# Kernel tuning notes

Hardware: AMD Instinct MI355X
Metric: run time of the kernel (lower is better)

Reference implementation:

```python
import jax, jax.numpy as jnp
import numpy as np

NUM_HEAD = 16
MODEL_DIM = 1024
K_DIM = MODEL_DIM // NUM_HEAD
LN_EPS = 1e-5


def setup_inputs() -> dict:
    key = jax.random.key(0)
    ks = jax.random.split(key, 9)
    B, N, D = 4, 2048, MODEL_DIM
    scale = 1.0 / np.sqrt(D)
    return {
        "q": jax.random.normal(ks[0], (B, N, D), dtype=jnp.float32),
        "k": jax.random.normal(ks[1], (B, N, D), dtype=jnp.float32),
        "v": jax.random.normal(ks[2], (B, N, D), dtype=jnp.float32),
        "Wq": jax.random.normal(ks[3], (D, D), dtype=jnp.float32) * scale,
        "Wk": jax.random.normal(ks[4], (D, D), dtype=jnp.float32) * scale,
        "Wv": jax.random.normal(ks[5], (D, D), dtype=jnp.float32) * scale,
        "Wo": jax.random.normal(ks[6], (D, D), dtype=jnp.float32) * scale,
        "gamma": jnp.ones((D,), dtype=jnp.float32),
        "beta": jnp.zeros((D,), dtype=jnp.float32),
    }


def reference(q, k, v, Wq, Wk, Wv, Wo, gamma, beta):
    B, N, D = q.shape
    H, Dh = NUM_HEAD, K_DIM
    # QKV projections (torch Linear: x @ W.T), then split heads -> [B,H,N,Dh]
    qs = (q @ Wq.T).reshape(B, N, H, Dh).transpose(0, 2, 1, 3)
    ks = (k @ Wk.T).reshape(B, N, H, Dh).transpose(0, 2, 1, 3)
    vs = (v @ Wv.T).reshape(B, N, H, Dh).transpose(0, 2, 1, 3)
    # scaled dot-product attention
    scores = jnp.einsum("bhqd,bhkd->bhqk", qs, ks) / jnp.sqrt(jnp.float32(Dh))
    probs = jax.nn.softmax(scores, axis=-1)
    attn = jnp.einsum("bhqk,bhkd->bhqd", probs, vs)
    # merge heads and output projection
    attn = attn.transpose(0, 2, 1, 3).reshape(B, N, D)
    out = attn @ Wo.T + q  # residual
    # LayerNorm
    mu = jnp.mean(out, axis=-1, keepdims=True)
    var = jnp.var(out, axis=-1, keepdims=True)
    out = (out - mu) * jax.lax.rsqrt(var + LN_EPS) * gamma + beta
    return out
```

## Files before the change

### kernel.cpp

```cpp
#include <hip/hip_runtime.h>
#include <cstdint>
#include <math.h>

typedef __bf16 bf16x8 __attribute__((ext_vector_type(8)));
typedef float f32x2 __attribute__((ext_vector_type(2)));
typedef float f32x4 __attribute__((ext_vector_type(4)));
typedef float f32x16 __attribute__((ext_vector_type(16)));
typedef int i32x2 __attribute__((ext_vector_type(2)));
typedef unsigned u32x4 __attribute__((ext_vector_type(4)));
typedef unsigned short u16;

#define B_ 4
#define N_ 2048
#define D_ 1024
#define H_ 16
#define DH_ 64
#define M_ (B_*N_)

#define QSCALE (0.125f * 1.44269504088896f)

typedef const void __attribute__((address_space(1))) gvoid;
typedef void __attribute__((address_space(3))) lvoid;

__device__ __forceinline__ void gload16(const void* g, void* l) {
  __builtin_amdgcn_global_load_lds((gvoid*)g, (lvoid*)l, 16, 0, 0);
}

__device__ __forceinline__ u16 cvt_bf(float f) {
  __bf16 h = (__bf16)f;
  return *(u16*)&h;
}

__device__ __forceinline__ unsigned cvt_pk(float lo, float hi) {
  unsigned r;
  asm("v_cvt_pk_bf16_f32 %0, %1, %2" : "=v"(r) : "v"(lo), "v"(hi));
  return r;
}

__device__ __forceinline__ i32x2 pl32swap(unsigned a, unsigned b) {
  return __builtin_amdgcn_permlane32_swap((int)a, (int)b, false, false);
}

__device__ __forceinline__ f32x2 pk_add(f32x2 a, f32x2 b) {
  f32x2 d;
  asm("v_pk_add_f32 %0, %1, %2" : "=v"(d) : "v"(a), "v"(b));
  return d;
}
__device__ __forceinline__ f32x2 pk_mul(f32x2 a, f32x2 b) {
  f32x2 d;
  asm("v_pk_mul_f32 %0, %1, %2" : "=v"(d) : "v"(a), "v"(b));
  return d;
}

__global__ __launch_bounds__(256) void cast_w(
    const float* __restrict__ a, const float* __restrict__ b,
    const float* __restrict__ c, const float* __restrict__ e,
    u16* __restrict__ oa, u16* __restrict__ ob, u16* __restrict__ oc, u16* __restrict__ oe) {
  const int nw = (D_*D_)/4;
  int i = blockIdx.x * 256 + threadIdx.x;
  const float* s; u16* d;
  if (i < nw)        { s = a; d = oa; }
  else if (i < 2*nw) { s = b; d = ob; i -= nw; }
  else if (i < 3*nw) { s = c; d = oc; i -= 2*nw; }
  else               { s = e; d = oe; i -= 3*nw; }
  float4 x = ((const float4*)s)[i];
  ushort4 y;
  y.x = cvt_bf(x.x); y.y = cvt_bf(x.y); y.z = cvt_bf(x.z); y.w = cvt_bf(x.w);
  ((ushort4*)d)[i] = y;
}

__global__ __launch_bounds__(256) void gemm_qkv(
    const float* __restrict__ Aq, const float* __restrict__ Ak, const float* __restrict__ Av,
    const u16* __restrict__ Wq, const u16* __restrict__ Wk, const u16* __restrict__ Wv,
    u16* __restrict__ Oq, u16* __restrict__ Ok, u16* __restrict__ Ov)
{
  __shared__ __align__(16) float As32[128*64];
  __shared__ __align__(16) u16 Bs[128*64];
  const int z = blockIdx.z;
  const float* A = (z == 0) ? Aq : (z == 1) ? Ak : Av;
  const u16* W  = (z == 0) ? Wq : (z == 1) ? Wk : Wv;
  u16* obf      = (z == 0) ? Oq : (z == 1) ? Ok : Ov;
  const float oscale = (z == 0) ? QSCALE : 1.0f;

  const int t = threadIdx.x;
  const int lane = t & 63;
  const int w = t >> 6;
  const int wr = w >> 1, wc = w & 1;
  const int m0 = blockIdx.x * 128;
  const int n0 = blockIdx.y * 128;
  f32x4 acc[4][4] = {};

  const int srow = t >> 3;
  const int scb = (t & 7) ^ (srow & 7);
  const int arow = t >> 4;
  const int asb  = (t & 15) ^ arow;

  const int fr = lane & 15;
  const int fg = lane >> 4;
  const int fs7 = fr & 7;

  for (int k0 = 0; k0 < 1024; k0 += 64) {
#pragma unroll
    for (int p = 0; p < 4; ++p)
      gload16(W + (size_t)(n0 + p*32 + srow)*1024 + k0 + scb*8, &Bs[(p*256 + t)*8]);
#pragma unroll
    for (int p = 0; p < 8; ++p)
      gload16(A + (size_t)(m0 + p*16 + arow)*1024 + k0 + asb*4, &As32[(p*256 + t)*4]);
    __syncthreads();
#pragma unroll
    for (int ks = 0; ks < 2; ++ks) {
      bf16x8 af[4], bfr[4];
#pragma unroll
      for (int i = 0; i < 4; ++i) {
        int ra = wr*64 + i*16 + fr;
        int b0 = (ks*4 + fg) * 2;
        int r15 = ra & 15;
        f32x4 lo = *(const f32x4*)&As32[ra*64 + ((b0 ^ r15) * 4)];
        f32x4 hi = *(const f32x4*)&As32[ra*64 + (((b0 + 1) ^ r15) * 4)];
        u32x4 pk = { cvt_pk(lo.x, lo.y), cvt_pk(lo.z, lo.w),
                     cvt_pk(hi.x, hi.y), cvt_pk(hi.z, hi.w) };
        af[i] = __builtin_bit_cast(bf16x8, pk);
        int rb = wc*64 + i*16 + fr;
        bfr[i] = *(const bf16x8*)&Bs[rb*64 + (((ks*4 + fg) ^ fs7) * 8)];
      }
#pragma unroll
      for (int i = 0; i < 4; ++i)
#pragma unroll
        for (int j = 0; j < 4; ++j)
          acc[i][j] = __builtin_amdgcn_mfma_f32_16x16x32_bf16(af[i], bfr[j], acc[i][j], 0, 0, 0);
    }
    __syncthreads();
  }

#pragma unroll
  for (int i = 0; i < 4; ++i) {
#pragma unroll
    for (int j = 0; j < 4; ++j) {
#pragma unroll
      for (int jj = 0; jj < 4; ++jj) {
        int row = m0 + wr*64 + i*16 + fg*4 + jj;
        int col = n0 + wc*64 + j*16 + fr;
        float val = acc[i][j][jj];
        int b = row >> 11, n = row & 2047, h = col >> 6, dh = col & 63;
        if (z != 2) {
          obf[(((size_t)(b*H_ + h))*N_ + n)*DH_ + dh] = cvt_bf(val * oscale);
        } else {
          obf[(((size_t)(b*H_ + h))*DH_ + dh)*N_ + n] = cvt_bf(val);
        }
      }
    }
  }
}

__global__ __launch_bounds__(256) void gemm_out(
    const u16* __restrict__ A, const u16* __restrict__ W,
    const float* __restrict__ resid, float* __restrict__ ofp)
{
  __shared__ __align__(16) u16 As[128*64];
  __shared__ __align__(16) u16 Bs[128*64];
  const int t = threadIdx.x;
  const int lane = t & 63;
  const int w = t >> 6;
  const int wr = w >> 1, wc = w & 1;
  const int m0 = blockIdx.x * 128;
  const int n0 = blockIdx.y * 128;
  f32x4 acc[4][4] = {};

  const int srow = t >> 3;
  const int scb = (t & 7) ^ (srow & 7);
  const int fr = lane & 15;
  const int fg = lane >> 4;
  const int fs7 = fr & 7;

  for (int k0 = 0; k0 < 1024; k0 += 64) {
#pragma unroll
    for (int p = 0; p < 4; ++p) {
      int r = p*32 + srow;
      gload16(A + (size_t)(m0 + r)*1024 + k0 + scb*8, &As[(p*256 + t)*8]);
      gload16(W + (size_t)(n0 + r)*1024 + k0 + scb*8, &Bs[(p*256 + t)*8]);
    }
    __syncthreads();
#pragma unroll
    for (int ks = 0; ks < 2; ++ks) {
      bf16x8 af[4], bfr[4];
#pragma unroll
      for (int i = 0; i < 4; ++i) {
        int ra = wr*64 + i*16 + fr;
        af[i]  = *(const bf16x8*)&As[ra*64 + (((ks*4 + fg) ^ fs7) * 8)];
        int rb = wc*64 + i*16 + fr;
        bfr[i] = *(const bf16x8*)&Bs[rb*64 + (((ks*4 + fg) ^ fs7) * 8)];
      }
#pragma unroll
      for (int i = 0; i < 4; ++i)
#pragma unroll
        for (int j = 0; j < 4; ++j)
          acc[i][j] = __builtin_amdgcn_mfma_f32_16x16x32_bf16(af[i], bfr[j], acc[i][j], 0, 0, 0);
    }
    __syncthreads();
  }

#pragma unroll
  for (int i = 0; i < 4; ++i)
#pragma unroll
    for (int j = 0; j < 4; ++j)
#pragma unroll
      for (int jj = 0; jj < 4; ++jj) {
        int row = m0 + wr*64 + i*16 + fg*4 + jj;
        int col = n0 + wc*64 + j*16 + fr;
        size_t idx = (size_t)row*1024 + col;
        ofp[idx] = acc[i][j][jj] + resid[idx];
      }
}

__device__ __forceinline__ f32x2 sp2(const f32x16& S, int i) {
  f32x2 r; r.x = S[2*i]; r.y = S[2*i + 1]; return r;
}
__device__ __forceinline__ void exp2v(f32x16& S) {
#pragma unroll
  for (int r = 0; r < 16; ++r) S[r] = __builtin_amdgcn_exp2f(S[r]);
}
__device__ __forceinline__ f32x2 sumtree(const f32x16& S0, const f32x16& S1) {
  f32x2 a0 = pk_add(sp2(S0,0), sp2(S0,1));
  f32x2 a1 = pk_add(sp2(S0,2), sp2(S0,3));
  f32x2 a2 = pk_add(sp2(S0,4), sp2(S0,5));
  f32x2 a3 = pk_add(sp2(S0,6), sp2(S0,7));
  f32x2 b0 = pk_add(sp2(S1,0), sp2(S1,1));
  f32x2 b1 = pk_add(sp2(S1,2), sp2(S1,3));
  f32x2 b2 = pk_add(sp2(S1,4), sp2(S1,5));
  f32x2 b3 = pk_add(sp2(S1,6), sp2(S1,7));
  a0 = pk_add(a0, a1); a2 = pk_add(a2, a3);
  b0 = pk_add(b0, b1); b2 = pk_add(b2, b3);
  a0 = pk_add(a0, a2); b0 = pk_add(b0, b2);
  return pk_add(a0, b0);
}
__device__ __forceinline__ void buildP(const f32x16& S, bf16x8* pf) {
  unsigned w0 = cvt_pk(S[0], S[1]),  w1 = cvt_pk(S[2], S[3]);
  unsigned w2 = cvt_pk(S[4], S[5]),  w3 = cvt_pk(S[6], S[7]);
  i32x2 A2 = pl32swap(w0, w2), B2 = pl32swap(w1, w3);
  u32x4 f0 = { (unsigned)A2.x, (unsigned)B2.x, (unsigned)A2.y, (unsigned)B2.y };
  pf[0] = __builtin_bit_cast(bf16x8, f0);
  unsigned w4 = cvt_pk(S[8], S[9]),   w5 = cvt_pk(S[10], S[11]);
  unsigned w6 = cvt_pk(S[12], S[13]), w7 = cvt_pk(S[14], S[15]);
  i32x2 C2 = pl32swap(w4, w6), D2 = pl32swap(w5, w7);
  u32x4 f1 = { (unsigned)C2.x, (unsigned)D2.x, (unsigned)C2.y, (unsigned)D2.y };
  pf[1] = __builtin_bit_cast(bf16x8, f1);
}

__global__ __launch_bounds__(256, 2) void flash_attn(
    const u16* __restrict__ Qs, const u16* __restrict__ Ks,
    const u16* __restrict__ VTs, u16* __restrict__ ctx)
{
  __shared__ __align__(16) u16 Klds[2][128*64];
  __shared__ __align__(16) u16 Vlds[2][64*128];
  const int t = threadIdx.x;
  const int lane = t & 63;
  const int w = t >> 6;
  const int l31 = lane & 31;
  const int h = lane >> 5;
  const int bh = blockIdx.x;
  const int q0 = blockIdx.y * 256 + w * 64;
  const u16* Qbh = Qs  + (size_t)bh * N_ * DH_;
  const u16* Kbh = Ks  + (size_t)bh * N_ * DH_;
  const u16* Vbh = VTs + (size_t)bh * DH_ * N_;

  bf16x8 qfA[4], qfB[4];
#pragma unroll
  for (int dd = 0; dd < 4; ++dd) {
    qfA[dd] = *(const bf16x8*)&Qbh[(size_t)(q0 + l31)*64 + dd*16 + h*8];
    qfB[dd] = *(const bf16x8*)&Qbh[(size_t)(q0 + 32 + l31)*64 + dd*16 + h*8];
  }

  f32x2 lA = {0.f, 0.f}, lB = {0.f, 0.f};
  f32x16 OA0 = {}, OA1 = {}, OB0 = {}, OB1 = {};

  const int krow = t >> 3;
  const int kcb  = (t & 7) ^ (krow & 7);
  const int vrow = t >> 4;
  const int vcb  = (t & 15) ^ vrow;
  const u16* ksrc = Kbh + (size_t)krow*64 + kcb*8;
  const u16* vsrc = Vbh + (size_t)vrow*N_ + vcb*8;

  auto stage = [&](int buf, int kv) {
#pragma unroll
    for (int p = 0; p < 4; ++p)
      gload16(ksrc + (size_t)(kv + p*32)*64, &Klds[buf][(p*256 + t)*8]);
#pragma unroll
    for (int p = 0; p < 4; ++p)
      gload16(vsrc + kv + (size_t)(p*16)*N_, &Vlds[buf][(p*256 + t)*8]);
  };

  const int l7 = l31 & 7;
  const int l15 = l31 & 15;

  stage(0, 0);
  __syncthreads();
  int cur = 0;

  for (int kv0 = 0; kv0 < N_; kv0 += 128) {
    if (kv0 + 128 < N_) stage(cur ^ 1, kv0 + 128);

#pragma unroll
    for (int c = 0; c < 2; ++c) {
      const int kb = c * 64;
      bf16x8 kf0[4], kf1[4];
#pragma unroll
      for (int dd = 0; dd < 4; ++dd) {
        int cb = ((dd*2 + h) ^ l7) * 8;
        kf0[dd] = *(const bf16x8*)&Klds[cur][(kb + l31)*64 + cb];
        kf1[dd] = *(const bf16x8*)&Klds[cur][(kb + 32 + l31)*64 + cb];
      }
      bf16x8 vf0[4], vf1[4];
#pragma unroll
      for (int ks = 0; ks < 4; ++ks) {
        int kc = (c*8 + ks*2 + h) ^ l15;
        vf0[ks] = *(const bf16x8*)&Vlds[cur][l31*128 + kc*8];
        vf1[ks] = *(const bf16x8*)&Vlds[cur][(32 + l31)*128 + kc*8];
      }

      f32x16 SA0 = {}, SA1 = {}, SB0 = {}, SB1 = {};
#pragma unroll
      for (int dd = 0; dd < 4; ++dd) {
        SA0 = __builtin_amdgcn_mfma_f32_32x32x16_bf16(kf0[dd], qfA[dd], SA0, 0, 0, 0);
        SA1 = __builtin_amdgcn_mfma_f32_32x32x16_bf16(kf1[dd], qfA[dd], SA1, 0, 0, 0);
      }
#pragma unroll
      for (int dd = 0; dd < 4; ++dd) {
        SB0 = __builtin_amdgcn_mfma_f32_32x32x16_bf16(kf0[dd], qfB[dd], SB0, 0, 0, 0);
        SB1 = __builtin_amdgcn_mfma_f32_32x32x16_bf16(kf1[dd], qfB[dd], SB1, 0, 0, 0);
      }

      exp2v(SA0); exp2v(SA1);
      bf16x8 pfA[4];
      buildP(SA0, &pfA[0]);
      buildP(SA1, &pfA[2]);

#pragma unroll
      for (int ks = 0; ks < 4; ++ks) {
        OA0 = __builtin_amdgcn_mfma_f32_32x32x16_bf16(vf0[ks], pfA[ks], OA0, 0, 0, 0);
        OA1 = __builtin_amdgcn_mfma_f32_32x32x16_bf16(vf1[ks], pfA[ks], OA1, 0, 0, 0);
      }
      lA = pk_add(lA, sumtree(SA0, SA1));

      exp2v(SB0); exp2v(SB1);
      bf16x8 pfB[4];
      buildP(SB0, &pfB[0]);
      buildP(SB1, &pfB[2]);
#pragma unroll
      for (int ks = 0; ks < 4; ++ks) {
        OB0 = __builtin_amdgcn_mfma_f32_32x32x16_bf16(vf0[ks], pfB[ks], OB0, 0, 0, 0);
        OB1 = __builtin_amdgcn_mfma_f32_32x32x16_bf16(vf1[ks], pfB[ks], OB1, 0, 0, 0);
      }
      lB = pk_add(lB, sumtree(SB0, SB1));
    }

    __syncthreads();
    cur ^= 1;
  }

  int b = bh >> 4, hh = bh & 15;
  {
    float lps = lA.x + lA.y;
    i32x2 lsw = pl32swap(__float_as_uint(lps), __float_as_uint(lps));
    float ltot = __uint_as_float((unsigned)lsw.x) + __uint_as_float((unsigned)lsw.y);
    float linv = __builtin_amdgcn_rcpf(ltot);
    f32x2 li2; li2.x = linv; li2.y = linv;
    unsigned* crow = (unsigned*)(ctx + ((size_t)b*N_ + (q0 + l31))*D_ + hh*64);
#pragma unroll
    for (int rp = 0; rp < 8; ++rp) {
      int r = rp*2;
      int d0 = (r & 3) + 8*(r >> 2) + 4*h;
      f32x2 o0 = pk_mul(sp2(OA0, rp), li2);
      f32x2 o1 = pk_mul(sp2(OA1, rp), li2);
      crow[d0 >> 1]        = cvt_pk(o0.x, o0.y);
      crow[(d0 + 32) >> 1] = cvt_pk(o1.x, o1.y);
    }
  }
  {
    float lps = lB.x + lB.y;
    i32x2 lsw = pl32swap(__float_as_uint(lps), __float_as_uint(lps));
    float ltot = __uint_as_float((unsigned)lsw.x) + __uint_as_float((unsigned)lsw.y);
    float linv = __builtin_amdgcn_rcpf(ltot);
    f32x2 li2; li2.x = linv; li2.y = linv;
    unsigned* crow = (unsigned*)(ctx + ((size_t)b*N_ + (q0 + 32 + l31))*D_ + hh*64);
#pragma unroll
    for (int rp = 0; rp < 8; ++rp) {
      int r = rp*2;
      int d0 = (r & 3) + 8*(r >> 2) + 4*h;
      f32x2 o0 = pk_mul(sp2(OB0, rp), li2);
      f32x2 o1 = pk_mul(sp2(OB1, rp), li2);
      crow[d0 >> 1]        = cvt_pk(o0.x, o0.y);
      crow[(d0 + 32) >> 1] = cvt_pk(o1.x, o1.y);
    }
  }
}

__global__ __launch_bounds__(256) void ln_fwd(float* __restrict__ io,
    const float* __restrict__ gamma, const float* __restrict__ beta)
{
  __shared__ float red[4];
  const int t = threadIdx.x;
  const int lane = t & 63, w = t >> 6;
  float4* row = (float4*)(io + (size_t)blockIdx.x * 1024);
  float4 x = row[t];
  float s = x.x + x.y + x.z + x.w;
#pragma unroll
  for (int m = 1; m < 64; m <<= 1) s += __shfl_xor(s, m);
  if (lane == 0) red[w] = s;
  __syncthreads();
  float mean = (red[0] + red[1] + red[2] + red[3]) * (1.f/1024.f);
  __syncthreads();
  float dx0 = x.x - mean, dx1 = x.y - mean, dx2 = x.z - mean, dx3 = x.w - mean;
  float sq = dx0*dx0 + dx1*dx1 + dx2*dx2 + dx3*dx3;
#pragma unroll
  for (int m = 1; m < 64; m <<= 1) sq += __shfl_xor(sq, m);
  if (lane == 0) red[w] = sq;
  __syncthreads();
  float var = (red[0] + red[1] + red[2] + red[3]) * (1.f/1024.f);
  float rstd = rsqrtf(var + 1e-5f);
  float4 g = ((const float4*)gamma)[t];
  float4 bb = ((const float4*)beta)[t];
  float4 y;
  y.x = dx0*rstd*g.x + bb.x;
  y.y = dx1*rstd*g.y + bb.y;
  y.z = dx2*rstd*g.z + bb.z;
  y.w = dx3*rstd*g.w + bb.w;
  row[t] = y;
}

extern "C" void kernel_launch(void* const* d_in, const int* in_sizes, int n_in,
                              void* d_out, int out_size, void* d_ws, size_t ws_size,
                              hipStream_t stream) {
  const float* q     = (const float*)d_in[0];
  const float* k     = (const float*)d_in[1];
  const float* v     = (const float*)d_in[2];
  const float* Wq    = (const float*)d_in[3];
  const float* Wk    = (const float*)d_in[4];
  const float* Wv    = (const float*)d_in[5];
  const float* Wo    = (const float*)d_in[6];
  const float* gamma = (const float*)d_in[7];
  const float* beta  = (const float*)d_in[8];
  float* out = (float*)d_out;

  char* ws = (char*)d_ws;
  const size_t MB = 1024*1024;
  u16* Wqb = (u16*)(ws + 0*MB);
  u16* Wkb = (u16*)(ws + 2*MB);
  u16* Wvb = (u16*)(ws + 4*MB);
  u16* Wob = (u16*)(ws + 6*MB);
  u16* Qs  = (u16*)(ws + 8*MB);
  u16* Ks  = (u16*)(ws + 24*MB);
  u16* VTs = (u16*)(ws + 40*MB);
  u16* ctx = (u16*)(ws + 56*MB);

  const int nw4 = 4*((D_*D_)/4);
  cast_w<<<nw4/256, 256, 0, stream>>>(Wq, Wk, Wv, Wo, Wqb, Wkb, Wvb, Wob);

  dim3 gproj(M_/128, D_/128, 3);
  gemm_qkv<<<gproj, 256, 0, stream>>>(q, k, v, Wqb, Wkb, Wvb, Qs, Ks, VTs);

  flash_attn<<<dim3(B_*H_, N_/256), 256, 0, stream>>>(Qs, Ks, VTs, ctx);

  gemm_out<<<dim3(M_/128, D_/128), 256, 0, stream>>>(ctx, Wob, q, out);

  ln_fwd<<<M_, 256, 0, stream>>>(out, gamma, beta);
}
```

Before: 209.5 us.

## Prefetch next K tile in QKV GEMM and convert activations to bf16 before LDS

Measured after the change: 223.6 us. +6.8%, slower.

```diff
diff --git a/kernel.cpp b/kernel.cpp
--- a/kernel.cpp
+++ b/kernel.cpp
@@ -74,8 +74,8 @@
     const u16* __restrict__ Wq, const u16* __restrict__ Wk, const u16* __restrict__ Wv,
     u16* __restrict__ Oq, u16* __restrict__ Ok, u16* __restrict__ Ov)
 {
-  __shared__ __align__(16) float As32[128*64];
-  __shared__ __align__(16) u16 Bs[128*64];
+  __shared__ __align__(16) u16 As[128*64];
+  __shared__ __align__(16) u16 Bs[2][128*64];
   const int z = blockIdx.z;
   const float* A = (z == 0) ? Aq : (z == 1) ? Ak : Av;
   const u16* W  = (z == 0) ? Wq : (z == 1) ? Wk : Wv;
@@ -90,38 +90,64 @@
   const int n0 = blockIdx.y * 128;
   f32x4 acc[4][4] = {};
 
+  const int arow0 = t >> 3;
+  const int acb   = t & 7;
+  const float* asrc = A + (size_t)(m0 + arow0)*1024 + acb*8;
   const int srow = t >> 3;
-  const int scb = (t & 7) ^ (srow & 7);
-  const int arow = t >> 4;
-  const int asb  = (t & 15) ^ arow;
+  const int scb  = (t & 7) ^ (srow & 7);
+  const u16* wsrc = W + (size_t)(n0 + srow)*1024 + scb*8;
 
   const int fr = lane & 15;
   const int fg = lane >> 4;
   const int fs7 = fr & 7;
 
+  float4 areg[8];
+  auto aload = [&](int k0) {
+#pragma unroll
+    for (int p = 0; p < 4; ++p) {
+      const float* s = asrc + (size_t)(p*32)*1024 + k0;
+      areg[2*p]   = *(const float4*)s;
+      areg[2*p+1] = *(const float4*)(s + 4);
+    }
+  };
+  auto awrite = [&]() {
+#pragma unroll
+    for (int p = 0; p < 4; ++p) {
+      int row = p*32 + arow0;
+      u32x4 pk = { cvt_pk(areg[2*p].x,   areg[2*p].y),
+                   cvt_pk(areg[2*p].z,   areg[2*p].w),
+                   cvt_pk(areg[2*p+1].x, areg[2*p+1].y),
+                   cvt_pk(areg[2*p+1].z, areg[2*p+1].w) };
+      *(u32x4*)&As[row*64 + ((acb ^ (row & 7)) * 8)] = pk;
+    }
+  };
+  auto wstage = [&](int buf, int k0) {
+#pragma unroll
+    for (int p = 0; p < 4; ++p)
+      gload16(wsrc + (size_t)(p*32)*1024 + k0, &Bs[buf][(p*256 + t)*8]);
+  };
+
+  aload(0);
+  wstage(0, 0);
+  awrite();
+  __syncthreads();
+  int cur = 0;
+
   for (int k0 = 0; k0 < 1024; k0 += 64) {
-#pragma unroll
-    for (int p = 0; p < 4; ++p)
-      gload16(W + (size_t)(n0 + p*32 + srow)*1024 + k0 + scb*8, &Bs[(p*256 + t)*8]);
-#pragma unroll
-    for (int p = 0; p < 8; ++p)
-      gload16(A + (size_t)(m0 + p*16 + arow)*1024 + k0 + asb*4, &As32[(p*256 + t)*4]);
-    __syncthreads();
+    const bool more = (k0 + 64 < 1024);
+    if (more) {
+      aload(k0 + 64);
+      wstage(cur ^ 1, k0 + 64);
+    }
 #pragma unroll
     for (int ks = 0; ks < 2; ++ks) {
       bf16x8 af[4], bfr[4];
 #pragma unroll
       for (int i = 0; i < 4; ++i) {
         int ra = wr*64 + i*16 + fr;
-        int b0 = (ks*4 + fg) * 2;
-        int r15 = ra & 15;
-        f32x4 lo = *(const f32x4*)&As32[ra*64 + ((b0 ^ r15) * 4)];
-        f32x4 hi = *(const f32x4*)&As32[ra*64 + (((b0 + 1) ^ r15) * 4)];
-        u32x4 pk = { cvt_pk(lo.x, lo.y), cvt_pk(lo.z, lo.w),
-                     cvt_pk(hi.x, hi.y), cvt_pk(hi.z, hi.w) };
-        af[i] = __builtin_bit_cast(bf16x8, pk);
+        af[i]  = *(const bf16x8*)&As[ra*64 + (((ks*4 + fg) ^ (ra & 7)) * 8)];
         int rb = wc*64 + i*16 + fr;
-        bfr[i] = *(const bf16x8*)&Bs[rb*64 + (((ks*4 + fg) ^ fs7) * 8)];
+        bfr[i] = *(const bf16x8*)&Bs[cur][rb*64 + (((ks*4 + fg) ^ fs7) * 8)];
       }
 #pragma unroll
       for (int i = 0; i < 4; ++i)
@@ -130,6 +156,11 @@
           acc[i][j] = __builtin_amdgcn_mfma_f32_16x16x32_bf16(af[i], bfr[j], acc[i][j], 0, 0, 0);
     }
     __syncthreads();
+    if (more) {
+      awrite();
+      __syncthreads();
+    }
+    cur ^= 1;
   }
 
 #pragma unroll
```
